# Performance work log

Hardware: AMD Instinct MI355X
Metric: run time of the kernel (lower is better)

The kernel has to match this reference:

```python
import jax, jax.numpy as jnp
import numpy as np

B, S, D = 2, 2048, 1024
H, DH = 16, 64  # num_heads, hidden_dimension (per-head)


def setup_inputs() -> dict:
    key = jax.random.key(0)
    ks = jax.random.split(key, 9)
    s = 1.0 / np.sqrt(D)
    so = 1.0 / np.sqrt(H * DH)
    return {
        "x": jax.random.normal(ks[0], (B, S, D), dtype=jnp.float32),
        "Wq": jax.random.uniform(ks[1], (D, H * DH), jnp.float32, -s, s),
        "bq": jax.random.uniform(ks[2], (H * DH,), jnp.float32, -s, s),
        "Wk": jax.random.uniform(ks[3], (D, H * DH), jnp.float32, -s, s),
        "bk": jax.random.uniform(ks[4], (H * DH,), jnp.float32, -s, s),
        "Wv": jax.random.uniform(ks[5], (D, H * DH), jnp.float32, -s, s),
        "bv": jax.random.uniform(ks[6], (H * DH,), jnp.float32, -s, s),
        "Wo": jax.random.uniform(ks[7], (H * DH, D), jnp.float32, -so, so),
        "bo": jax.random.uniform(ks[8], (D,), jnp.float32, -so, so),
    }


def reference(x, Wq, bq, Wk, bk, Wv, bv, Wo, bo):
    b, s, _ = x.shape
    # project and split heads: [b, h, s, dh]
    q = (x @ Wq + bq).reshape(b, s, H, DH).transpose(0, 2, 1, 3)
    k = (x @ Wk + bk).reshape(b, s, H, DH).transpose(0, 2, 1, 3)
    v = (x @ Wv + bv).reshape(b, s, H, DH).transpose(0, 2, 1, 3)
    scores = jnp.einsum('bhqd,bhkd->bhqk', q, k) / jnp.sqrt(jnp.float32(DH))
    causal = jnp.triu(jnp.ones((s, s), dtype=bool), k=1)
    scores = jnp.where(causal, -jnp.inf, scores)
    weights = jax.nn.softmax(scores, axis=-1)
    out = jnp.einsum('bhqk,bhkd->bhqd', weights, v)
    out = out.transpose(0, 2, 1, 3).reshape(b, s, H * DH)
    return out @ Wo + bo
```

## Files before the change

### kernel.cpp

```cpp
#include <hip/hip_runtime.h>

#define B_  2
#define S_  2048
#define D_  1024
#define H_  16
#define DH_ 64
#define NDH (H_*DH_)
#define BS_ (B_*S_)
#define PER ((size_t)B_*H_*S_*DH_)

typedef __bf16 bf16;
typedef bf16 bf16x8 __attribute__((ext_vector_type(8)));
typedef bf16 bf16x4 __attribute__((ext_vector_type(4)));
typedef float f32x4 __attribute__((ext_vector_type(4)));

#define AS1 __attribute__((address_space(1)))
#define AS3 __attribute__((address_space(3)))
__device__ inline void gld16(const bf16* g, bf16* l) {
    __builtin_amdgcn_global_load_lds((const AS1 void*)g, (AS3 void*)l, 16, 0, 0);
}

__global__ __launch_bounds__(256) void prep(
        const float* __restrict__ x,
        const float* __restrict__ W0, const float* __restrict__ W1,
        const float* __restrict__ W2, const float* __restrict__ W3,
        bf16* __restrict__ xb, bf16* __restrict__ T0, bf16* __restrict__ T1,
        bf16* __restrict__ T2, bf16* __restrict__ T3) {
    __shared__ float T[32][33];
    int bid = blockIdx.x, t = threadIdx.x;
    if (bid < 4096) {
        int i = (bid * 256 + t) * 4;
        float4 v = *(const float4*)(x + i);
        bf16x4 o = { (bf16)v.x, (bf16)v.y, (bf16)v.z, (bf16)v.w };
        *(bf16x4*)(xb + i) = o;
        return;
    }
    int r2 = bid - 4096;
    int z = r2 >> 10, w = r2 & 1023;
    const float* W = (z == 0) ? W0 : (z == 1) ? W1 : (z == 2) ? W2 : W3;
    bf16* Wt = (z == 0) ? T0 : (z == 1) ? T1 : (z == 2) ? T2 : T3;
    int k0 = (w >> 5) * 32, n0 = (w & 31) * 32;
    int r = t >> 3, c = (t & 7) * 4;
    float4 v = *(const float4*)(W + (size_t)(k0 + r) * 1024 + n0 + c);
    T[c + 0][r] = v.x; T[c + 1][r] = v.y; T[c + 2][r] = v.z; T[c + 3][r] = v.w;
    __syncthreads();
    bf16x4 o = { (bf16)T[r][c], (bf16)T[r][c + 1], (bf16)T[r][c + 2], (bf16)T[r][c + 3] };
    *(bf16x4*)(Wt + (size_t)(n0 + r) * 1024 + k0 + c) = o;
}

__global__ __launch_bounds__(256) void qkv_gemm(
        const bf16* __restrict__ A, const bf16* __restrict__ Bt,
        const float* __restrict__ bq, const float* __restrict__ bk,
        const float* __restrict__ bv, bf16* __restrict__ Qout, bf16* __restrict__ Vt) {
    __shared__ __align__(16) bf16 As[128 * 32];
    __shared__ __align__(16) bf16 Bs[128 * 32];
    int tid = threadIdx.x, wave = tid >> 6, lane = tid & 63;
    int quad = lane >> 4, l16 = lane & 15;
    int bm = blockIdx.y * 128, bn = blockIdx.x * 128;
    int wm = (wave >> 1) * 64, wn = (wave & 1) * 64;

    int sr = lane >> 2, sc = (lane & 3) * 8;
    const bf16* Ag0 = A + (size_t)(bm + (wave * 2 + 0) * 16 + sr) * 1024 + sc;
    const bf16* Ag1 = A + (size_t)(bm + (wave * 2 + 1) * 16 + sr) * 1024 + sc;
    const bf16* Bg0 = Bt + (size_t)(bn + (wave * 2 + 0) * 16 + sr) * 1024 + sc;
    const bf16* Bg1 = Bt + (size_t)(bn + (wave * 2 + 1) * 16 + sr) * 1024 + sc;
    bf16* Al0 = &As[(wave * 2 + 0) * 512];
    bf16* Al1 = &As[(wave * 2 + 1) * 512];
    bf16* Bl0 = &Bs[(wave * 2 + 0) * 512];
    bf16* Bl1 = &Bs[(wave * 2 + 1) * 512];

    f32x4 acc[4][4] = {};

    for (int k0 = 0; k0 < 1024; k0 += 32) {
        gld16(Ag0 + k0, Al0);
        gld16(Ag1 + k0, Al1);
        gld16(Bg0 + k0, Bl0);
        gld16(Bg1 + k0, Bl1);
        __syncthreads();
        bf16x8 af[4], bfr[4];
        #pragma unroll
        for (int i = 0; i < 4; ++i)
            af[i] = *(const bf16x8*)&As[(wm + i * 16 + l16) * 32 + quad * 8];
        #pragma unroll
        for (int j = 0; j < 4; ++j)
            bfr[j] = *(const bf16x8*)&Bs[(wn + j * 16 + l16) * 32 + quad * 8];
        #pragma unroll
        for (int i = 0; i < 4; ++i)
          #pragma unroll
          for (int j = 0; j < 4; ++j)
            acc[i][j] = __builtin_amdgcn_mfma_f32_16x16x32_bf16(af[i], bfr[j], acc[i][j], 0, 0, 0);
        __syncthreads();
    }

    #pragma unroll
    for (int i = 0; i < 4; ++i)
      #pragma unroll
      for (int j = 0; j < 4; ++j) {
        int col = bn + wn + j * 16 + l16;
        float bias = (col < 1024) ? bq[col] : (col < 2048) ? bk[col - 1024] : bv[col - 2048];
        int qkv = col >> 10, cw = col & 1023;
        int hh = cw >> 6, d = cw & 63;
        int row0 = bm + wm + i * 16 + quad * 4;
        int bb = row0 >> 11, s0 = row0 & 2047;
        if (qkv < 2) {
            #pragma unroll
            for (int r = 0; r < 4; ++r)
                Qout[(size_t)qkv * PER + (((size_t)bb * H_ + hh) * S_ + s0 + r) * DH_ + d] =
                    (bf16)(acc[i][j][r] + bias);
        } else {
            bf16x4 pack;
            #pragma unroll
            for (int r = 0; r < 4; ++r) pack[r] = (bf16)(acc[i][j][r] + bias);
            *(bf16x4*)&Vt[(((size_t)bb * H_ + hh) * DH_ + d) * S_ + s0] = pack;
        }
      }
}

__global__ __launch_bounds__(256) void gemm128f(
        const bf16* __restrict__ A, const bf16* __restrict__ Bt,
        const float* __restrict__ bias, float* __restrict__ out) {
    __shared__ __align__(16) bf16 As[128 * 32];
    __shared__ __align__(16) bf16 Bs[128 * 32];
    int tid = threadIdx.x, wave = tid >> 6, lane = tid & 63;
    int quad = lane >> 4, l16 = lane & 15;
    int bm = blockIdx.y * 128, bn = blockIdx.x * 128;
    int wm = (wave >> 1) * 64, wn = (wave & 1) * 64;

    int sr = lane >> 2, sc = (lane & 3) * 8;
    const bf16* Ag0 = A + (size_t)(bm + (wave * 2 + 0) * 16 + sr) * 1024 + sc;
    const bf16* Ag1 = A + (size_t)(bm + (wave * 2 + 1) * 16 + sr) * 1024 + sc;
    const bf16* Bg0 = Bt + (size_t)(bn + (wave * 2 + 0) * 16 + sr) * 1024 + sc;
    const bf16* Bg1 = Bt + (size_t)(bn + (wave * 2 + 1) * 16 + sr) * 1024 + sc;
    bf16* Al0 = &As[(wave * 2 + 0) * 512];
    bf16* Al1 = &As[(wave * 2 + 1) * 512];
    bf16* Bl0 = &Bs[(wave * 2 + 0) * 512];
    bf16* Bl1 = &Bs[(wave * 2 + 1) * 512];

    f32x4 acc[4][4] = {};

    for (int k0 = 0; k0 < 1024; k0 += 32) {
        gld16(Ag0 + k0, Al0);
        gld16(Ag1 + k0, Al1);
        gld16(Bg0 + k0, Bl0);
        gld16(Bg1 + k0, Bl1);
        __syncthreads();
        bf16x8 af[4], bfr[4];
        #pragma unroll
        for (int i = 0; i < 4; ++i)
            af[i] = *(const bf16x8*)&As[(wm + i * 16 + l16) * 32 + quad * 8];
        #pragma unroll
        for (int j = 0; j < 4; ++j)
            bfr[j] = *(const bf16x8*)&Bs[(wn + j * 16 + l16) * 32 + quad * 8];
        #pragma unroll
        for (int i = 0; i < 4; ++i)
          #pragma unroll
          for (int j = 0; j < 4; ++j)
            acc[i][j] = __builtin_amdgcn_mfma_f32_16x16x32_bf16(af[i], bfr[j], acc[i][j], 0, 0, 0);
        __syncthreads();
    }

    #pragma unroll
    for (int i = 0; i < 4; ++i)
      #pragma unroll
      for (int j = 0; j < 4; ++j) {
        int col = bn + wn + j * 16 + l16;
        float b = bias[col];
        #pragma unroll
        for (int r = 0; r < 4; ++r) {
            int row = bm + wm + i * 16 + quad * 4 + r;
            out[(size_t)row * 1024 + col] = acc[i][j][r] + b;
        }
      }
}

__global__ __launch_bounds__(256) void flash4(
        const bf16* __restrict__ Q, const bf16* __restrict__ K,
        const bf16* __restrict__ Vt, bf16* __restrict__ O) {
    int bh = blockIdx.x;
    int b = bh >> 4, h = bh & 15;
    int pr = blockIdx.y;
    int tid = threadIdx.x;
    int wave = tid >> 6, lane = tid & 63;
    int quad = lane >> 4, l16 = lane & 15;

    __shared__ __align__(16) char smem[4 * 2 * 16 * 72 * 2];
    bf16 (*P)[2][16][72] = reinterpret_cast<bf16 (*)[2][16][72]>(smem);
    float (*redO)[4][64][4] = reinterpret_cast<float (*)[4][64][4]>(smem);
    __shared__ float redL[4][2][4][4];

    const bf16* Qb = Q + (size_t)bh * S_ * DH_;
    const bf16* Kb = K + (size_t)bh * S_ * DH_;
    const bf16* Vb = Vt + (size_t)bh * DH_ * S_;

    bf16x8 ones;
    #pragma unroll
    for (int j = 0; j < 8; ++j) ones[j] = (l16 == 0) ? (bf16)1.0f : (bf16)0.0f;

    for (int half = 0; half < 2; ++half) {
        int tile = half ? (63 - pr) : pr;
        int q0 = tile * 32;

        bf16x8 qf[2][2];
        #pragma unroll
        for (int s = 0; s < 2; ++s) {
            const bf16* qp = Qb + (size_t)(q0 + s * 16 + l16) * DH_ + quad * 8;
            qf[s][0] = *(const bf16x8*)(qp);
            qf[s][1] = *(const bf16x8*)(qp + 32);
        }

        f32x4 oacc[2][4] = {};
        f32x4 lacc[2] = {};

        int nkt = tile / 2 + 1;
        for (int kt = wave; kt < nkt; kt += 4) {
            int kv0 = kt * 64;
            bf16x8 kf[4][2];
            #pragma unroll
            for (int ns = 0; ns < 4; ++ns) {
                const bf16* kp = Kb + (size_t)(kv0 + ns * 16 + l16) * DH_ + quad * 8;
                kf[ns][0] = *(const bf16x8*)(kp);
                kf[ns][1] = *(const bf16x8*)(kp + 32);
            }
            f32x4 sacc[2][4] = {};
            #pragma unroll
            for (int s = 0; s < 2; ++s)
              #pragma unroll
              for (int ns = 0; ns < 4; ++ns) {
                sacc[s][ns] = __builtin_amdgcn_mfma_f32_16x16x32_bf16(qf[s][0], kf[ns][0], sacc[s][ns], 0, 0, 0);
                sacc[s][ns] = __builtin_amdgcn_mfma_f32_16x16x32_bf16(qf[s][1], kf[ns][1], sacc[s][ns], 0, 0, 0);
              }
            bool diag = (kt == nkt - 1);
            #pragma unroll
            for (int s = 0; s < 2; ++s)
              #pragma unroll
              for (int ns = 0; ns < 4; ++ns)
                #pragma unroll
                for (int r = 0; r < 4; ++r) {
                    float p = __expf(sacc[s][ns][r] * 0.125f);
                    if (diag) {
                        int kv = kv0 + ns * 16 + l16;
                        int qq = q0 + s * 16 + quad * 4 + r;
                        if (kv > qq) p = 0.f;
                    }
                    P[wave][s][quad * 4 + r][ns * 16 + l16] = (bf16)p;
                }
            #pragma unroll
            for (int ks = 0; ks < 2; ++ks) {
                bf16x8 pf0 = *(const bf16x8*)&P[wave][0][l16][ks * 32 + quad * 8];
                bf16x8 pf1 = *(const bf16x8*)&P[wave][1][l16][ks * 32 + quad * 8];
                lacc[0] = __builtin_amdgcn_mfma_f32_16x16x32_bf16(pf0, ones, lacc[0], 0, 0, 0);
                lacc[1] = __builtin_amdgcn_mfma_f32_16x16x32_bf16(pf1, ones, lacc[1], 0, 0, 0);
                #pragma unroll
                for (int ds = 0; ds < 4; ++ds) {
                    bf16x8 vf = *(const bf16x8*)(Vb + (size_t)(ds * 16 + l16) * S_ + kv0 + ks * 32 + quad * 8);
                    oacc[0][ds] = __builtin_amdgcn_mfma_f32_16x16x32_bf16(pf0, vf, oacc[0][ds], 0, 0, 0);
                    oacc[1][ds] = __builtin_amdgcn_mfma_f32_16x16x32_bf16(pf1, vf, oacc[1][ds], 0, 0, 0);
                }
            }
        }

        if (l16 == 0) {
            #pragma unroll
            for (int s = 0; s < 2; ++s)
              #pragma unroll
              for (int r = 0; r < 4; ++r)
                redL[wave][s][quad][r] = lacc[s][r];
        }
        #pragma unroll
        for (int s = 0; s < 2; ++s) {
            __syncthreads();
            #pragma unroll
            for (int ds = 0; ds < 4; ++ds)
                *(f32x4*)&redO[wave][ds][lane][0] = oacc[s][ds];
            __syncthreads();
            f32x4 osum = {};
            #pragma unroll
            for (int w = 0; w < 4; ++w)
                osum += *(const f32x4*)&redO[w][wave][lane][0];
            #pragma unroll
            for (int r = 0; r < 4; ++r) {
                float lsum = redL[0][s][quad][r] + redL[1][s][quad][r]
                           + redL[2][s][quad][r] + redL[3][s][quad][r];
                int qq = q0 + s * 16 + quad * 4 + r;
                O[((size_t)b * S_ + qq) * NDH + h * DH_ + wave * 16 + l16] = (bf16)(osum[r] / lsum);
            }
        }
        __syncthreads();
    }
}

extern "C" void kernel_launch(void* const* d_in, const int* in_sizes, int n_in,
                              void* d_out, int out_size, void* d_ws, size_t ws_size,
                              hipStream_t stream) {
    const float* x  = (const float*)d_in[0];
    const float* Wq = (const float*)d_in[1];
    const float* bq = (const float*)d_in[2];
    const float* Wk = (const float*)d_in[3];
    const float* bk = (const float*)d_in[4];
    const float* Wv = (const float*)d_in[5];
    const float* bv = (const float*)d_in[6];
    const float* Wo = (const float*)d_in[7];
    const float* bo = (const float*)d_in[8];
    float* out = (float*)d_out;

    bf16* ws = (bf16*)d_ws;
    const size_t M1 = (size_t)1024 * 1024;
    bf16* xb    = ws;
    bf16* WqkvT = ws + 4 * M1;
    bf16* WoT   = ws + 7 * M1;
    bf16* Qw    = ws + 8 * M1;
    bf16* Vtw   = ws + 16 * M1;
    bf16* Ow    = ws + 20 * M1;

    prep<<<8192, 256, 0, stream>>>(x, Wq, Wk, Wv, Wo,
                                   xb, WqkvT, WqkvT + M1, WqkvT + 2 * M1, WoT);

    qkv_gemm<<<dim3(3072 / 128, BS_ / 128), 256, 0, stream>>>(xb, WqkvT, bq, bk, bv, Qw, Vtw);

    flash4<<<dim3(B_ * H_, 32), 256, 0, stream>>>(Qw, Qw + PER, Vtw, Ow);

    gemm128f<<<dim3(1024 / 128, BS_ / 128), 256, 0, stream>>>(Ow, WoT, bo, out);
}
```

Baseline: 220.3 us.

## Double-buffer GEMM LDS loads, swizzle tiles, fold softmax scale into Q

Both GEMMs now double-buffer their LDS tiles, prefetching the next K-slice with global_load_lds while MFMAs run on the current one, so each iteration needs one barrier instead of two. Block indices are remapped with a swizzle for better L2 locality. The output projection moves to 128x64 tiles to launch more blocks. Q is pre-scaled by log2(e)/sqrt(64) so the softmax can use a raw exp2 in place of a multiply plus expf. This uses twice the LDS per block and changes Q's bf16 rounding slightly.

```diff
diff --git a/kernel.cpp b/kernel.cpp
--- a/kernel.cpp
+++ b/kernel.cpp
@@ -13,6 +13,8 @@
 typedef bf16 bf16x8 __attribute__((ext_vector_type(8)));
 typedef bf16 bf16x4 __attribute__((ext_vector_type(4)));
 typedef float f32x4 __attribute__((ext_vector_type(4)));
+
+#define QSCALE 0.18033688011112042f
 
 #define AS1 __attribute__((address_space(1)))
 #define AS3 __attribute__((address_space(3)))
@@ -52,11 +54,14 @@
         const bf16* __restrict__ A, const bf16* __restrict__ Bt,
         const float* __restrict__ bq, const float* __restrict__ bk,
         const float* __restrict__ bv, bf16* __restrict__ Qout, bf16* __restrict__ Vt) {
-    __shared__ __align__(16) bf16 As[128 * 32];
-    __shared__ __align__(16) bf16 Bs[128 * 32];
+    __shared__ __align__(16) bf16 As[2][128 * 32];
+    __shared__ __align__(16) bf16 Bs[2][128 * 32];
     int tid = threadIdx.x, wave = tid >> 6, lane = tid & 63;
     int quad = lane >> 4, l16 = lane & 15;
-    int bm = blockIdx.y * 128, bn = blockIdx.x * 128;
+
+    int flat = blockIdx.y * 24 + blockIdx.x;
+    int swz  = (flat & 7) * 96 + (flat >> 3);
+    int bm = (swz / 24) * 128, bn = (swz % 24) * 128;
     int wm = (wave >> 1) * 64, wn = (wave & 1) * 64;
 
     int sr = lane >> 2, sc = (lane & 3) * 8;
@@ -64,32 +69,41 @@
     const bf16* Ag1 = A + (size_t)(bm + (wave * 2 + 1) * 16 + sr) * 1024 + sc;
     const bf16* Bg0 = Bt + (size_t)(bn + (wave * 2 + 0) * 16 + sr) * 1024 + sc;
     const bf16* Bg1 = Bt + (size_t)(bn + (wave * 2 + 1) * 16 + sr) * 1024 + sc;
-    bf16* Al0 = &As[(wave * 2 + 0) * 512];
-    bf16* Al1 = &As[(wave * 2 + 1) * 512];
-    bf16* Bl0 = &Bs[(wave * 2 + 0) * 512];
-    bf16* Bl1 = &Bs[(wave * 2 + 1) * 512];
+    int la0 = (wave * 2 + 0) * 512;
+    int la1 = (wave * 2 + 1) * 512;
 
     f32x4 acc[4][4] = {};
 
-    for (int k0 = 0; k0 < 1024; k0 += 32) {
-        gld16(Ag0 + k0, Al0);
-        gld16(Ag1 + k0, Al1);
-        gld16(Bg0 + k0, Bl0);
-        gld16(Bg1 + k0, Bl1);
-        __syncthreads();
+    gld16(Ag0, &As[0][la0]);
+    gld16(Ag1, &As[0][la1]);
+    gld16(Bg0, &Bs[0][la0]);
+    gld16(Bg1, &Bs[0][la1]);
+    asm volatile("s_waitcnt vmcnt(0)" ::: "memory");
+    __builtin_amdgcn_s_barrier();
+
+    for (int t = 0; t < 32; ++t) {
+        int cur = t & 1, nxt = cur ^ 1;
+        if (t < 31) {
+            int k0 = (t + 1) * 32;
+            gld16(Ag0 + k0, &As[nxt][la0]);
+            gld16(Ag1 + k0, &As[nxt][la1]);
+            gld16(Bg0 + k0, &Bs[nxt][la0]);
+            gld16(Bg1 + k0, &Bs[nxt][la1]);
+        }
         bf16x8 af[4], bfr[4];
         #pragma unroll
         for (int i = 0; i < 4; ++i)
-            af[i] = *(const bf16x8*)&As[(wm + i * 16 + l16) * 32 + quad * 8];
+            af[i] = *(const bf16x8*)&As[cur][(wm + i * 16 + l16) * 32 + quad * 8];
         #pragma unroll
         for (int j = 0; j < 4; ++j)
-            bfr[j] = *(const bf16x8*)&Bs[(wn + j * 16 + l16) * 32 + quad * 8];
+            bfr[j] = *(const bf16x8*)&Bs[cur][(wn + j * 16 + l16) * 32 + quad * 8];
         #pragma unroll
         for (int i = 0; i < 4; ++i)
           #pragma unroll
           for (int j = 0; j < 4; ++j)
             acc[i][j] = __builtin_amdgcn_mfma_f32_16x16x32_bf16(af[i], bfr[j], acc[i][j], 0, 0, 0);
-        __syncthreads();
+        asm volatile("s_waitcnt vmcnt(0)" ::: "memory");
+        __builtin_amdgcn_s_barrier();
     }
 
     #pragma unroll
@@ -103,10 +117,11 @@
         int row0 = bm + wm + i * 16 + quad * 4;
         int bb = row0 >> 11, s0 = row0 & 2047;
         if (qkv < 2) {
+            float scl = (qkv == 0) ? QSCALE : 1.0f;
             #pragma unroll
             for (int r = 0; r < 4; ++r)
                 Qout[(size_t)qkv * PER + (((size_t)bb * H_ + hh) * S_ + s0 + r) * DH_ + d] =
-                    (bf16)(acc[i][j][r] + bias);
+                    (bf16)((acc[i][j][r] + bias) * scl);
         } else {
             bf16x4 pack;
             #pragma unroll
@@ -116,53 +131,63 @@
       }
 }
 
-__global__ __launch_bounds__(256) void gemm128f(
+__global__ __launch_bounds__(256) void gemm_proj(
         const bf16* __restrict__ A, const bf16* __restrict__ Bt,
         const float* __restrict__ bias, float* __restrict__ out) {
-    __shared__ __align__(16) bf16 As[128 * 32];
-    __shared__ __align__(16) bf16 Bs[128 * 32];
+    __shared__ __align__(16) bf16 As[2][128 * 32];
+    __shared__ __align__(16) bf16 Bs[2][64 * 32];
     int tid = threadIdx.x, wave = tid >> 6, lane = tid & 63;
     int quad = lane >> 4, l16 = lane & 15;
-    int bm = blockIdx.y * 128, bn = blockIdx.x * 128;
-    int wm = (wave >> 1) * 64, wn = (wave & 1) * 64;
+
+    int flat = blockIdx.y * 16 + blockIdx.x;
+    int swz  = (flat & 7) * 64 + (flat >> 3);
+    int bm = (swz / 16) * 128, bn = (swz % 16) * 64;
+    int wm = (wave >> 1) * 64, wn = (wave & 1) * 32;
 
     int sr = lane >> 2, sc = (lane & 3) * 8;
     const bf16* Ag0 = A + (size_t)(bm + (wave * 2 + 0) * 16 + sr) * 1024 + sc;
     const bf16* Ag1 = A + (size_t)(bm + (wave * 2 + 1) * 16 + sr) * 1024 + sc;
-    const bf16* Bg0 = Bt + (size_t)(bn + (wave * 2 + 0) * 16 + sr) * 1024 + sc;
-    const bf16* Bg1 = Bt + (size_t)(bn + (wave * 2 + 1) * 16 + sr) * 1024 + sc;
-    bf16* Al0 = &As[(wave * 2 + 0) * 512];
-    bf16* Al1 = &As[(wave * 2 + 1) * 512];
-    bf16* Bl0 = &Bs[(wave * 2 + 0) * 512];
-    bf16* Bl1 = &Bs[(wave * 2 + 1) * 512];
-
-    f32x4 acc[4][4] = {};
-
-    for (int k0 = 0; k0 < 1024; k0 += 32) {
-        gld16(Ag0 + k0, Al0);
-        gld16(Ag1 + k0, Al1);
-        gld16(Bg0 + k0, Bl0);
-        gld16(Bg1 + k0, Bl1);
-        __syncthreads();
-        bf16x8 af[4], bfr[4];
+    const bf16* Bg0 = Bt + (size_t)(bn + wave * 16 + sr) * 1024 + sc;
+    int la0 = (wave * 2 + 0) * 512;
+    int la1 = (wave * 2 + 1) * 512;
+    int lb0 = wave * 512;
+
+    f32x4 acc[4][2] = {};
+
+    gld16(Ag0, &As[0][la0]);
+    gld16(Ag1, &As[0][la1]);
+    gld16(Bg0, &Bs[0][lb0]);
+    asm volatile("s_waitcnt vmcnt(0)" ::: "memory");
+    __builtin_amdgcn_s_barrier();
+
+    for (int t = 0; t < 32; ++t) {
+        int cur = t & 1, nxt = cur ^ 1;
+        if (t < 31) {
+            int k0 = (t + 1) * 32;
+            gld16(Ag0 + k0, &As[nxt][la0]);
+            gld16(Ag1 + k0, &As[nxt][la1]);
+            gld16(Bg0 + k0, &Bs[nxt][lb0]);
+        }
+        bf16x8 af[4], bfr[2];
         #pragma unroll
         for (int i = 0; i < 4; ++i)
-            af[i] = *(const bf16x8*)&As[(wm + i * 16 + l16) * 32 + quad * 8];
-        #pragma unroll
-        for (int j = 0; j < 4; ++j)
-            bfr[j] = *(const bf16x8*)&Bs[(wn + j * 16 + l16) * 32 + quad * 8];
+            af[i] = *(const bf16x8*)&As[cur][(wm + i * 16 + l16) * 32 + quad * 8];
+        #pragma unroll
+        for (int j = 0; j < 2; ++j)
+            bfr[j] = *(const bf16x8*)&Bs[cur][(wn + j * 16 + l16) * 32 + quad * 8];
         #pragma unroll
         for (int i = 0; i < 4; ++i)
           #pragma unroll
-          for (int j = 0; j < 4; ++j)
+          for (int j = 0; j < 2; ++j)
             acc[i][j] = __builtin_amdgcn_mfma_f32_16x16x32_bf16(af[i], bfr[j], acc[i][j], 0, 0, 0);
-        __syncthreads();
+        asm volatile("s_waitcnt vmcnt(0)" ::: "memory");
+        __builtin_amdgcn_s_barrier();
     }
 
     #pragma unroll
     for (int i = 0; i < 4; ++i)
       #pragma unroll
-      for (int j = 0; j < 4; ++j) {
+      for (int j = 0; j < 2; ++j) {
         int col = bn + wn + j * 16 + l16;
         float b = bias[col];
         #pragma unroll
@@ -236,7 +261,7 @@
               for (int ns = 0; ns < 4; ++ns)
                 #pragma unroll
                 for (int r = 0; r < 4; ++r) {
-                    float p = __expf(sacc[s][ns][r] * 0.125f);
+                    float p = __builtin_amdgcn_exp2f(sacc[s][ns][r]);
                     if (diag) {
                         int kv = kv0 + ns * 16 + l16;
                         int qq = q0 + s * 16 + quad * 4 + r;
@@ -319,5 +344,5 @@
 
     flash4<<<dim3(B_ * H_, 32), 256, 0, stream>>>(Qw, Qw + PER, Vtw, Ow);
 
-    gemm128f<<<dim3(1024 / 128, BS_ / 128), 256, 0, stream>>>(Ow, WoT, bo, out);
-}
+    gemm_proj<<<dim3(1024 / 64, BS_ / 128), 256, 0, stream>>>(Ow, WoT, bo, out);
+}
```

After: 220.0 us. No clear change (-0.1%).
